# Kernel tuning notes

Hardware: AMD Instinct MI355X
Metric: run time of the kernel (lower is better)

## Reference

```python
import jax, jax.numpy as jnp
import numpy as np

MIN_NORM = 1e-15
BALL_EPS = 4e-3  # hgcn PoincareBall eps for float32
C = 1.0          # c_in = c_out = 1


def _artanh(x):
    return jnp.arctanh(jnp.clip(x, -1.0 + 1e-7, 1.0 - 1e-7))


def _norm(x):
    return jnp.clip(jnp.linalg.norm(x, axis=-1, keepdims=True), MIN_NORM)


def proj(x, c=C):
    n = _norm(x)
    maxnorm = (1.0 - BALL_EPS) / jnp.sqrt(c)
    return jnp.where(n > maxnorm, x / n * maxnorm, x)


def expmap0(u, c=C):
    sc = jnp.sqrt(c)
    n = _norm(u)
    return jnp.tanh(sc * n) * u / (sc * n)


def logmap0(p, c=C):
    sc = jnp.sqrt(c)
    n = _norm(p)
    return _artanh(sc * n) * p / (sc * n)


def mobius_add(x, y, c=C):
    x2 = jnp.sum(x * x, -1, keepdims=True)
    y2 = jnp.sum(y * y, -1, keepdims=True)
    xy = jnp.sum(x * y, -1, keepdims=True)
    num = (1 + 2 * c * xy + c * y2) * x + (1 - c * x2) * y
    den = 1 + 2 * c * xy + c * c * x2 * y2
    return num / jnp.clip(den, MIN_NORM)


def mobius_matvec(m, x, c=C):
    # m: [out, in] torch-Linear layout; mx = x @ m.T
    sc = jnp.sqrt(c)
    xn = _norm(x)
    mx = x @ m.T
    mxn = _norm(mx)
    res = jnp.tanh(mxn / xn * _artanh(sc * xn)) * mx / (mxn * sc)
    zero = jnp.all(mx == 0, axis=-1, keepdims=True)
    return jnp.where(zero, jnp.zeros_like(res), res)


def hyp_linear(x, w, b, c=C):
    res = proj(mobius_matvec(w, x, c), c)
    hyp_bias = proj(expmap0(b[None, :], c), c)  # proj_tan0 is identity on Poincare ball
    return proj(mobius_add(res, hyp_bias, c), c)


def hyp_act(x, c_in=C, c_out=C):
    xt = jax.nn.relu(logmap0(x, c_in))
    return proj(expmap0(xt, c_out), c_out)


def mean_agg(h, src, dst, n):
    # mean of source-node features over incoming edges per destination node
    s = jax.ops.segment_sum(h[src], dst, num_segments=n)
    deg = jax.ops.segment_sum(jnp.ones((src.shape[0],), h.dtype), dst, num_segments=n)
    return s / jnp.clip(deg, 1.0)[:, None]


def setup_inputs() -> dict:
    key = jax.random.key(0)
    N, D, E = 100000, 128, 1600000  # in_features = out_features = 128
    ks = jax.random.split(key, 20)
    inp = {
        "x": jax.random.normal(ks[0], (N, D), jnp.float32) * 0.01,  # keep near ball origin
        "src_pos": jax.random.randint(ks[1], (E,), 0, N, jnp.int32),
        "dst_pos": jax.random.randint(ks[2], (E,), 0, N, jnp.int32),
        "src_neg": jax.random.randint(ks[3], (E,), 0, N, jnp.int32),
        "dst_neg": jax.random.randint(ks[4], (E,), 0, N, jnp.int32),
    }
    s = 0.01
    inp["W1b"] = jax.random.normal(ks[5], (D, 2 * D), jnp.float32) * s
    inp["b1b"] = jax.random.normal(ks[6], (D,), jnp.float32) * s
    inp["W1h"] = jax.random.normal(ks[7], (D, 2 * D), jnp.float32) * s
    inp["b1h"] = jax.random.normal(ks[8], (D,), jnp.float32) * s
    inp["W2b"] = jax.random.normal(ks[9], (2 * D, 3 * D), jnp.float32) * s
    inp["b2b"] = jax.random.normal(ks[10], (2 * D,), jnp.float32) * s
    inp["W2h"] = jax.random.normal(ks[11], (2 * D, 3 * D), jnp.float32) * s
    inp["b2h"] = jax.random.normal(ks[12], (2 * D,), jnp.float32) * s
    inp["W3b"] = jax.random.normal(ks[13], (D, 2 * D), jnp.float32) * s
    inp["b3b"] = jax.random.normal(ks[14], (D,), jnp.float32) * s
    inp["W3h"] = jax.random.normal(ks[15], (D, 2 * D), jnp.float32) * s
    inp["b3h"] = jax.random.normal(ks[16], (D,), jnp.float32) * s
    return inp


def reference(x, src_pos, dst_pos, src_neg, dst_neg,
              W1b, b1b, W1h, b1h, W2b, b2b, W2h, b2h, W3b, b3b, W3h, b3h):
    n = x.shape[0]
    # layer-1 signed neighbor means over x
    pos1 = mean_agg(x, src_pos, dst_pos, n)
    neg1 = mean_agg(x, src_neg, dst_neg, n)
    h_b1 = hyp_act(hyp_linear(jnp.concatenate([pos1, x], axis=1), W1b, b1b))
    h_n1 = hyp_act(hyp_linear(jnp.concatenate([neg1, x], axis=1), W1h, b1h))
    # layer-2 balance-theory aggregation over (h_b1, h_n1)
    pos2 = jnp.concatenate([mean_agg(h_b1, src_pos, dst_pos, n),
                            mean_agg(h_n1, src_neg, dst_neg, n)], axis=1)
    neg2 = jnp.concatenate([mean_agg(h_n1, src_pos, dst_pos, n),
                            mean_agg(h_b1, src_neg, dst_neg, n)], axis=1)
    h_b2 = hyp_act(hyp_linear(jnp.concatenate([pos2, h_b1], axis=1), W2b, b2b))
    h_n2 = hyp_act(hyp_linear(jnp.concatenate([neg2, h_n1], axis=1), W2h, b2h))
    h_b3 = hyp_act(hyp_linear(h_b2, W3b, b3b))
    h_n3 = hyp_act(hyp_linear(h_n2, W3h, b3h))
    return jnp.concatenate([h_b3, h_n3, x], axis=1)  # [N, 3*D]
```

## Files before the change

kernel.cpp:

```cpp
#include <hip/hip_runtime.h>
#include <cstdint>
#include <cstddef>

#define DEV __device__ __forceinline__

typedef unsigned int uint32;
typedef unsigned short ushort16;
typedef __bf16 bfx8 __attribute__((ext_vector_type(8)));
typedef float f32x4 __attribute__((ext_vector_type(4)));

constexpr int D = 128;
constexpr int CAP = 64;
constexpr float MINN  = 1e-15f;
constexpr float MAXN  = 1.0f - 4e-3f;
constexpr float ACLIP = 1.0f - 1e-7f;

DEV float wave_sum(float v) {
#pragma unroll
  for (int off = 32; off > 0; off >>= 1) v += __shfl_xor(v, off, 64);
  return v;
}

DEV float artanh_clip(float x) {
  x = fminf(x, ACLIP);
  return 0.5f * logf((1.0f + x) / (1.0f - x));
}

DEV uint32 f2b(float f) {
  uint32 u = __float_as_uint(f);
  u += 0x7fffu + ((u >> 16) & 1u);
  return u >> 16;
}
DEV float b2f_lo(uint32 v) { return __uint_as_float(v << 16); }
DEV float b2f_hi(uint32 v) { return __uint_as_float(v & 0xffff0000u); }

__global__ __launch_bounds__(256) void fillc_k(
    const int* __restrict__ sp, const int* __restrict__ dp,
    const int* __restrict__ sn, const int* __restrict__ dn, int E,
    int* __restrict__ cp, int* __restrict__ cn,
    int* __restrict__ lp, int* __restrict__ ln, int rngsz, int chunkE) {
  const int* __restrict__ src = blockIdx.y ? sn : sp;
  const int* __restrict__ dst = blockIdx.y ? dn : dp;
  int* __restrict__ cur = blockIdx.y ? cn : cp;
  int* __restrict__ lst = blockIdx.y ? ln : lp;
  const int r = blockIdx.x & 7;
  const int chunk = blockIdx.x >> 3;
  const unsigned lo = (unsigned)(r * rngsz);
  const int base = chunk * chunkE;
  const int end = min(base + chunkE, E);
  for (int i = base + (int)threadIdx.x; i < end; i += 256) {
    int d = dst[i];
    if ((unsigned)d - lo < (unsigned)rngsz) {
      int p = atomicAdd(&cur[d], 1);
      if (p < CAP) lst[(size_t)d * CAP + p] = src[i];
    }
  }
}

__global__ void rowsq_k(const float* __restrict__ x, float* __restrict__ xsq,
                        ushort16* __restrict__ xb, float* __restrict__ outx,
                        int* __restrict__ curz, int nz, int n) {
  int gid = blockIdx.x * 256 + (int)threadIdx.x;
  if (gid < nz) curz[gid] = 0;
  int lane = threadIdx.x & 63;
  int row = blockIdx.x * 4 + (threadIdx.x >> 6);
  if (row >= n) return;
  const float2 v = *(const float2*)(x + (size_t)row * D + lane * 2);
  uint32 pk = f2b(v.x) | (f2b(v.y) << 16);
  *(uint32*)(xb + (size_t)row * D + lane * 2) = pk;
  *(float2*)(outx + (size_t)row * 384 + 256 + lane * 2) = v;
  float s = wave_sum(v.x * v.x + v.y * v.y);
  if (lane == 0) xsq[row] = s;
}

struct BiasDesc { const float* b[6]; float* hb[6]; int dim[6]; };
__global__ void bias_all_k(BiasDesc bd, float* __restrict__ hbsq) {
  int i = blockIdx.x;
  int lane = threadIdx.x;
  const float* b = bd.b[i];
  float* hb = bd.hb[i];
  int ne = bd.dim[i] / 64;
  float v[4];
  float ssq = 0.0f;
  for (int e = 0; e < ne; ++e) { v[e] = b[e * 64 + lane]; ssq += v[e] * v[e]; }
  ssq = wave_sum(ssq);
  float nr = sqrtf(ssq);
  float nc = fmaxf(nr, MINN);
  float es = tanhf(nc) / nc;
  float on = es * nr;
  float f = (on > MAXN) ? (MAXN / fmaxf(on, MINN)) : 1.0f;
  float w = es * f;
  float osq = 0.0f;
  for (int e = 0; e < ne; ++e) { v[e] *= w; osq += v[e] * v[e]; hb[e * 64 + lane] = v[e]; }
  osq = wave_sum(osq);
  if (lane == 0) hbsq[i] = osq;
}

struct WsDesc { const float* src[6]; ushort16* dst[6]; int K[6]; int total[6]; };
__global__ void wshuf_all_k(WsDesc wd) {
  int y = blockIdx.y;
  int tid = blockIdx.x * 256 + threadIdx.x;
  if (tid >= wd.total[y]) return;
  int K = wd.K[y];
  int l = tid & 63;
  int fc = tid >> 6;
  int nkc = K / 32;
  int kc = fc % nkc;
  int jt = fc / nkc;
  int col = jt * 16 + (l & 15);
  int kb = kc * 32 + (l >> 4) * 8;
  const float* src = wd.src[y] + (size_t)col * K + kb;
  uint32 o[4];
#pragma unroll
  for (int m = 0; m < 4; ++m) o[m] = f2b(src[2 * m]) | (f2b(src[2 * m + 1]) << 16);
  *(uint4*)(wd.dst[y] + (size_t)tid * 8) = make_uint4(o[0], o[1], o[2], o[3]);
}

struct AggJob {
  const char* T;
  const int* cnt; const int* lst;
  ushort16* OutLo; ushort16* OutHi;
  float* Slo; float* Shi;
};

template <int NF>
__global__ __launch_bounds__(256) void agg2_k(AggJob ja, AggJob jbv, int n) {
  AggJob jb = blockIdx.y ? jbv : ja;
  const int l = threadIdx.x & 63;
  const int row = blockIdx.x * 4 + ((int)threadIdx.x >> 6);
  if (row >= n) return;
  const int cnt = jb.cnt[row];
  const int m = min(cnt, CAP);
  const int* __restrict__ lst = jb.lst + (size_t)row * CAP;
  const char* __restrict__ T = jb.T;
  float a0 = 0, a1 = 0, a2 = 0, a3 = 0;
  int j = 0;
  if (NF == 2) {
    const int off = l * 8;
    for (; j + 15 < m; j += 16) {
      uint2 v[16];
#pragma unroll
      for (int q = 0; q < 16; ++q)
        v[q] = *(const uint2*)(T + (size_t)lst[j + q] * 512 + off);
#pragma unroll
      for (int q = 0; q < 16; ++q) {
        a0 += b2f_lo(v[q].x); a1 += b2f_hi(v[q].x);
        a2 += b2f_lo(v[q].y); a3 += b2f_hi(v[q].y);
      }
    }
    for (; j + 3 < m; j += 4) {
      uint2 v[4];
#pragma unroll
      for (int q = 0; q < 4; ++q)
        v[q] = *(const uint2*)(T + (size_t)lst[j + q] * 512 + off);
#pragma unroll
      for (int q = 0; q < 4; ++q) {
        a0 += b2f_lo(v[q].x); a1 += b2f_hi(v[q].x);
        a2 += b2f_lo(v[q].y); a3 += b2f_hi(v[q].y);
      }
    }
    for (; j < m; ++j) {
      uint2 v = *(const uint2*)(T + (size_t)lst[j] * 512 + off);
      a0 += b2f_lo(v.x); a1 += b2f_hi(v.x);
      a2 += b2f_lo(v.y); a3 += b2f_hi(v.y);
    }
  } else {
    const int off = (l & 31) * 8;
    const int g = l >> 5;
    for (; j + 15 < m; j += 16) {
      uint2 v[8];
#pragma unroll
      for (int q = 0; q < 8; ++q)
        v[q] = *(const uint2*)(T + (size_t)lst[j + g + 2 * q] * 256 + off);
#pragma unroll
      for (int q = 0; q < 8; ++q) {
        a0 += b2f_lo(v[q].x); a1 += b2f_hi(v[q].x);
        a2 += b2f_lo(v[q].y); a3 += b2f_hi(v[q].y);
      }
    }
    for (; j + 1 < m; j += 2) {
      uint2 v = *(const uint2*)(T + (size_t)lst[j + g] * 256 + off);
      a0 += b2f_lo(v.x); a1 += b2f_hi(v.x);
      a2 += b2f_lo(v.y); a3 += b2f_hi(v.y);
    }
    if (j < m && g == 0) {
      uint2 v = *(const uint2*)(T + (size_t)lst[j] * 256 + off);
      a0 += b2f_lo(v.x); a1 += b2f_hi(v.x);
      a2 += b2f_lo(v.y); a3 += b2f_hi(v.y);
    }
    a0 += __shfl_xor(a0, 32, 64);
    a1 += __shfl_xor(a1, 32, 64);
    a2 += __shfl_xor(a2, 32, 64);
    a3 += __shfl_xor(a3, 32, 64);
  }
  float inv = 1.0f / fmaxf((float)cnt, 1.0f);
  a0 *= inv; a1 *= inv; a2 *= inv; a3 *= inv;
  float sq = a0 * a0 + a1 * a1 + a2 * a2 + a3 * a3;
#pragma unroll
  for (int o2 = 1; o2 < 32; o2 <<= 1) sq += __shfl_xor(sq, o2, 64);
  uint2 o;
  o.x = f2b(a0) | (f2b(a1) << 16);
  o.y = f2b(a2) | (f2b(a3) << 16);
  if (NF == 2) {
    ushort16* Out = (l < 32) ? jb.OutLo : jb.OutHi;
    *(uint2*)((char*)Out + (size_t)row * 256 + (l & 31) * 8) = o;
    if (l == 0) jb.Slo[row] = sq;
    if (l == 32) jb.Shi[row] = sq;
  } else {
    if (l < 32) *(uint2*)((char*)jb.OutLo + (size_t)row * 256 + l * 8) = o;
    if (l == 0) jb.Slo[row] = sq;
  }
}

struct GJob {
  const ushort16* p[3];
  int lda[3], ko[3];
  const ushort16* Wp;
  const float *xs0, *xs1, *xs2;
  const float *hb, *hbsq_p;
  ushort16 *ob0, *ob1; int ldob;
  float* outf; int ldof, ocol;
  float* hsq_out;
};

template <int NC, int NCT>
__global__ __launch_bounds__(256) void gemm3_k(GJob j0, GJob j1, int M) {
  GJob jb = blockIdx.y ? j1 : j0;
  __shared__ char As[16384];
  __shared__ float hbs[NCT * 64];
  __shared__ float redA[4][64][2];
  __shared__ float redB[4][64];
  __shared__ float rs[64][4];
  const int t = threadIdx.x;
  const int l = t & 63;
  const int w = t >> 6;
  const int brow = blockIdx.x * 64;
  constexpr int KC32 = NC * 4;
  const int srow = t >> 4;
  const int sco = t & 15;

  for (int c = t; c < NCT * 64; c += 256) hbs[c] = jb.hb[c];

  auto gaddr = [&](int c, int h) -> const uint4* {
    int gr = min(brow + srow + h * 16, M - 1);
    return (const uint4*)(jb.p[c] + jb.ko[c] + (size_t)gr * jb.lda[c] + sco * 8);
  };

  f32x4 acc[4][NCT] = {};
  uint4 rga[4];
#pragma unroll
  for (int h = 0; h < 4; ++h) rga[h] = *gaddr(0, h);

#pragma unroll
  for (int c = 0; c < NC; ++c) {
#pragma unroll
    for (int h = 0; h < 4; ++h) {
      int row = srow + h * 16;
      *(uint4*)(As + row * 256 + ((sco * 16) ^ ((row & 7) << 4))) = rga[h];
    }
    __syncthreads();
    if (c + 1 < NC) {
#pragma unroll
      for (int h = 0; h < 4; ++h) rga[h] = *gaddr(c + 1, h);
    }
#pragma unroll
    for (int ks = 0; ks < 4; ++ks) {
      const int kb = ks * 64 + (l >> 4) * 16;
      bfx8 a[4], b[NCT];
#pragma unroll
      for (int j = 0; j < NCT; ++j)
        b[j] = *(const bfx8*)(jb.Wp + ((size_t)((w * NCT + j) * KC32 + c * 4 + ks)) * 512 + l * 8);
#pragma unroll
      for (int i = 0; i < 4; ++i) {
        int row = i * 16 + (l & 15);
        a[i] = *(const bfx8*)(As + row * 256 + (kb ^ ((row & 7) << 4)));
      }
#pragma unroll
      for (int i = 0; i < 4; ++i)
#pragma unroll
        for (int j = 0; j < NCT; ++j)
          acc[i][j] = __builtin_amdgcn_mfma_f32_16x16x32_bf16(a[i], b[j], acc[i][j], 0, 0, 0);
    }
    __syncthreads();
  }

#pragma unroll
  for (int i = 0; i < 4; ++i)
#pragma unroll
    for (int r = 0; r < 4; ++r) {
      float s = 0.0f, xy = 0.0f;
#pragma unroll
      for (int j = 0; j < NCT; ++j) {
        float m = acc[i][j][r];
        int col = w * (NCT * 16) + j * 16 + (l & 15);
        s += m * m;
        xy += m * hbs[col];
      }
#pragma unroll
      for (int off = 1; off < 16; off <<= 1) {
        s += __shfl_xor(s, off, 64);
        xy += __shfl_xor(xy, off, 64);
      }
      if ((l & 15) == 0) {
        int row = i * 16 + (l >> 4) * 4 + r;
        redA[w][row][0] = s;
        redA[w][row][1] = xy;
      }
    }
  __syncthreads();

  if (t < 64 && brow + t < M) {
    float ssq = redA[0][t][0] + redA[1][t][0] + redA[2][t][0] + redA[3][t][0];
    float xyr = redA[0][t][1] + redA[1][t][1] + redA[2][t][1] + redA[3][t][1];
    float mxn_raw = sqrtf(ssq);
    float xnsq = jb.xs0[brow + t];
    if (jb.xs1) xnsq += jb.xs1[brow + t];
    if (jb.xs2) xnsq += jb.xs2[brow + t];
    float xn = fmaxf(sqrtf(xnsq), MINN);
    float mxn = fmaxf(mxn_raw, MINN);
    float scal = tanhf(mxn / xn * artanh_clip(xn)) / mxn;
    float rn_raw = scal * mxn_raw;
    if (rn_raw > MAXN) { scal *= MAXN / fmaxf(rn_raw, MINN); rn_raw = MAXN; }
    float xyv = scal * xyr;
    float x2 = rn_raw * rn_raw;
    float y2 = *jb.hbsq_p;
    float den = fmaxf(1.0f + 2.0f * xyv + x2 * y2, MINN);
    float ax = (1.0f + 2.0f * xyv + y2) / den;
    float ay = (1.0f - x2) / den;
    float vsq = scal * scal * ssq;
    float psq = fmaxf(ax * ax * vsq + 2.0f * ax * ay * xyv + ay * ay * y2, 0.0f);
    float pn_raw = sqrtf(psq);
    float f2s = (pn_raw > MAXN) ? (MAXN / fmaxf(pn_raw, MINN)) : 1.0f;
    pn_raw = fminf(pn_raw, MAXN);
    float pn = fmaxf(pn_raw, MINN);
    float la = artanh_clip(pn) / pn * f2s;
    rs[t][0] = scal * ax;
    rs[t][1] = ay;
    rs[t][2] = la;
  }
  __syncthreads();

#pragma unroll
  for (int i = 0; i < 4; ++i)
#pragma unroll
    for (int r = 0; r < 4; ++r) {
      int row = i * 16 + (l >> 4) * 4 + r;
      float c1 = rs[row][0], c2 = rs[row][1];
      float pp = 0.0f;
#pragma unroll
      for (int j = 0; j < NCT; ++j) {
        int col = w * (NCT * 16) + j * 16 + (l & 15);
        float p = c1 * acc[i][j][r] + c2 * hbs[col];
        p = fmaxf(p, 0.0f);
        acc[i][j][r] = p;
        pp += p * p;
      }
#pragma unroll
      for (int off = 1; off < 16; off <<= 1) pp += __shfl_xor(pp, off, 64);
      if ((l & 15) == 0) redB[w][row] = pp;
    }
  __syncthreads();

  if (t < 64 && brow + t < M) {
    float ppos = redB[0][t] + redB[1][t] + redB[2][t] + redB[3][t];
    float la = rs[t][2];
    float tsq = la * la * ppos;
    float tn_raw = sqrtf(tsq);
    float tnc = fmaxf(tn_raw, MINN);
    float es = tanhf(tnc) / tnc;
    float on_raw = es * tn_raw;
    float f3 = (on_raw > MAXN) ? (MAXN / fmaxf(on_raw, MINN)) : 1.0f;
    float wsc = es * f3;
    float g = wsc * la;
    rs[t][3] = g;
    if (jb.hsq_out) jb.hsq_out[brow + t] = g * g * ppos;
  }
  __syncthreads();

#pragma unroll
  for (int i = 0; i < 4; ++i)
#pragma unroll
    for (int r = 0; r < 4; ++r) {
      int row = i * 16 + (l >> 4) * 4 + r;
      int gr = brow + row;
      if (gr < M) {
        float g = rs[row][3];
#pragma unroll
        for (int j = 0; j < NCT; ++j) {
          int col = w * (NCT * 16) + j * 16 + (l & 15);
          float o = g * acc[i][j][r];
          if (jb.ob0) {
            ushort16* ob = (col < 128) ? jb.ob0 : jb.ob1;
            ob[(size_t)gr * jb.ldob + (col & 127)] = (ushort16)f2b(o);
          } else {
            jb.outf[(size_t)gr * jb.ldof + jb.ocol + col] = o;
          }
        }
      }
    }
}

extern "C" void kernel_launch(void* const* d_in, const int* in_sizes, int n_in,
                              void* d_out, int out_size, void* d_ws, size_t ws_size,
                              hipStream_t stream) {
  const float* x = (const float*)d_in[0];
  const int* src_pos = (const int*)d_in[1];
  const int* dst_pos = (const int*)d_in[2];
  const int* src_neg = (const int*)d_in[3];
  const int* dst_neg = (const int*)d_in[4];
  const float* W1b = (const float*)d_in[5];
  const float* b1b = (const float*)d_in[6];
  const float* W1h = (const float*)d_in[7];
  const float* b1h = (const float*)d_in[8];
  const float* W2b = (const float*)d_in[9];
  const float* b2b = (const float*)d_in[10];
  const float* W2h = (const float*)d_in[11];
  const float* b2h = (const float*)d_in[12];
  const float* W3b = (const float*)d_in[13];
  const float* b3b = (const float*)d_in[14];
  const float* W3h = (const float*)d_in[15];
  const float* b3h = (const float*)d_in[16];

  const int N = in_sizes[0] / D;
  const int E = in_sizes[1];

  int* iw = (int*)d_ws;
  size_t io = 0;
  int* cur_p = iw + io;  io += N;
  int* cur_n = iw + io;  io += N;
  int* lst_p = iw + io;  io += (size_t)N * CAP;
  int* lst_n = iw + io;  io += (size_t)N * CAP;
  io = (io + 63) & ~(size_t)63;

  float* fw = (float*)(iw + io);
  size_t fo = 0;
  float* xsq = fw + fo;    fo += N;
  float* hsq_b1 = fw + fo; fo += N;
  float* hsq_n1 = fw + fo; fo += N;
  float* hsq_b2 = fw + fo; fo += N;
  float* hsq_n2 = fw + fo; fo += N;
  float* ssq_p1 = fw + fo; fo += N;
  float* ssq_n1 = fw + fo; fo += N;
  float* ssq_pp = fw + fo; fo += N;
  float* ssq_np = fw + fo; fo += N;
  float* ssq_nn = fw + fo; fo += N;
  float* ssq_bn = fw + fo; fo += N;
  float* hbase = fw + fo;  fo += 1056;
  fo = (fo + 31) & ~(size_t)31;

  ushort16* SB = (ushort16*)(fw + fo);
  const size_t NSB = (size_t)N * D;
  ushort16* TA = SB;
  ushort16* H1 = SB + NSB;
  ushort16* TD = SB + 3 * NSB;
  ushort16* TE = SB + 4 * NSB;
  ushort16* TF = SB + 5 * NSB;
  ushort16* wb1b = SB + 6 * NSB;
  ushort16* wb1h = wb1b + 32768;
  ushort16* wb2b = wb1h + 32768;
  ushort16* wb2h = wb2b + 98304;
  ushort16* wb3b = wb2h + 98304;
  ushort16* wb3h = wb3b + 32768;

  float* outf = (float*)d_out;

  float* hb1b = hbase + 0;
  float* hb1h = hbase + 128;
  float* hb2b = hbase + 256;
  float* hb2h = hbase + 512;
  float* hb3b = hbase + 768;
  float* hb3h = hbase + 896;
  float* hbsq = hbase + 1024;

  const int grow = (N + 3) / 4;
  const int gf = (N + 63) / 64;
  const int rngsz = (N + 7) / 8;
  const int chunkE = (E + 255) / 256;
  const int gpart = 256 * 8;

  rowsq_k<<<grow, 256, 0, stream>>>(x, xsq, TA, outf, cur_p, 2 * N, N);
  fillc_k<<<dim3(gpart, 2), 256, 0, stream>>>(src_pos, dst_pos, src_neg, dst_neg, E,
                                              cur_p, cur_n, lst_p, lst_n, rngsz, chunkE);
  {
    BiasDesc bd;
    bd.b[0] = b1b; bd.hb[0] = hb1b; bd.dim[0] = 128;
    bd.b[1] = b1h; bd.hb[1] = hb1h; bd.dim[1] = 128;
    bd.b[2] = b2b; bd.hb[2] = hb2b; bd.dim[2] = 256;
    bd.b[3] = b2h; bd.hb[3] = hb2h; bd.dim[3] = 256;
    bd.b[4] = b3b; bd.hb[4] = hb3b; bd.dim[4] = 128;
    bd.b[5] = b3h; bd.hb[5] = hb3h; bd.dim[5] = 128;
    bias_all_k<<<6, 64, 0, stream>>>(bd, hbsq);
  }
  {
    WsDesc wd;
    wd.src[0] = W1b; wd.dst[0] = wb1b; wd.K[0] = 256; wd.total[0] = 8 * 8 * 64;
    wd.src[1] = W1h; wd.dst[1] = wb1h; wd.K[1] = 256; wd.total[1] = 8 * 8 * 64;
    wd.src[2] = W2b; wd.dst[2] = wb2b; wd.K[2] = 384; wd.total[2] = 16 * 12 * 64;
    wd.src[3] = W2h; wd.dst[3] = wb2h; wd.K[3] = 384; wd.total[3] = 16 * 12 * 64;
    wd.src[4] = W3b; wd.dst[4] = wb3b; wd.K[4] = 256; wd.total[4] = 8 * 8 * 64;
    wd.src[5] = W3h; wd.dst[5] = wb3h; wd.K[5] = 256; wd.total[5] = 8 * 8 * 64;
    wshuf_all_k<<<dim3(48, 6), 256, 0, stream>>>(wd);
  }

  {
    AggJob jp{(const char*)TA, cur_p, lst_p, TD, nullptr, ssq_p1, nullptr};
    AggJob jn{(const char*)TA, cur_n, lst_n, TE, nullptr, ssq_n1, nullptr};
    agg2_k<1><<<dim3(grow, 2), 256, 0, stream>>>(jp, jn, N);
  }
  {
    GJob ja{}, jh{};
    ja.p[0] = TD; ja.lda[0] = 128; ja.ko[0] = 0;
    ja.p[1] = TA; ja.lda[1] = 128; ja.ko[1] = 0;
    ja.Wp = wb1b; ja.xs0 = ssq_p1; ja.xs1 = xsq; ja.xs2 = nullptr;
    ja.hb = hb1b; ja.hbsq_p = hbsq + 0;
    ja.ob0 = H1; ja.ob1 = nullptr; ja.ldob = 256;
    ja.outf = nullptr; ja.ldof = 0; ja.ocol = 0; ja.hsq_out = hsq_b1;
    jh = ja;
    jh.p[0] = TE; jh.Wp = wb1h; jh.xs0 = ssq_n1;
    jh.hb = hb1h; jh.hbsq_p = hbsq + 1; jh.ob0 = H1 + 128; jh.hsq_out = hsq_n1;
    gemm3_k<2, 2><<<dim3(gf, 2), 256, 0, stream>>>(ja, jh, N);
  }

  {
    AggJob jp{(const char*)H1, cur_p, lst_p, TD, TE, ssq_pp, ssq_np};
    AggJob jn{(const char*)H1, cur_n, lst_n, TF, TA, ssq_bn, ssq_nn};
    agg2_k<2><<<dim3(grow, 2), 256, 0, stream>>>(jp, jn, N);
  }
  {
    GJob ja{}, jh{};
    ja.p[0] = TD; ja.lda[0] = 128; ja.ko[0] = 0;
    ja.p[1] = TA; ja.lda[1] = 128; ja.ko[1] = 0;
    ja.p[2] = H1; ja.lda[2] = 256; ja.ko[2] = 0;
    ja.Wp = wb2b; ja.xs0 = ssq_pp; ja.xs1 = ssq_nn; ja.xs2 = hsq_b1;
    ja.hb = hb2b; ja.hbsq_p = hbsq + 2;
    ja.ob0 = TD; ja.ob1 = TA; ja.ldob = 128;
    ja.outf = nullptr; ja.ldof = 0; ja.ocol = 0; ja.hsq_out = hsq_b2;
    jh = ja;
    jh.p[0] = TE; jh.p[1] = TF; jh.ko[2] = 128;
    jh.Wp = wb2h; jh.xs0 = ssq_np; jh.xs1 = ssq_bn; jh.xs2 = hsq_n1;
    jh.hb = hb2h; jh.hbsq_p = hbsq + 3;
    jh.ob0 = TE; jh.ob1 = TF; jh.hsq_out = hsq_n2;
    gemm3_k<3, 4><<<dim3(gf, 2), 256, 0, stream>>>(ja, jh, N);
  }

  {
    GJob ja{}, jh{};
    ja.p[0] = TD; ja.lda[0] = 128; ja.ko[0] = 0;
    ja.p[1] = TA; ja.lda[1] = 128; ja.ko[1] = 0;
    ja.Wp = wb3b; ja.xs0 = hsq_b2; ja.xs1 = nullptr; ja.xs2 = nullptr;
    ja.hb = hb3b; ja.hbsq_p = hbsq + 4;
    ja.ob0 = nullptr; ja.ob1 = nullptr; ja.ldob = 0;
    ja.outf = outf; ja.ldof = 3 * D; ja.ocol = 0; ja.hsq_out = nullptr;
    jh = ja;
    jh.p[0] = TE; jh.p[1] = TF;
    jh.Wp = wb3h; jh.xs0 = hsq_n2;
    jh.hb = hb3h; jh.hbsq_p = hbsq + 5; jh.ocol = 128;
    gemm3_k<2, 2><<<dim3(gf, 2), 256, 0, stream>>>(ja, jh, N);
  }
}
```

Baseline: 866.4 us.

## Split each aggregation row across two wavefronts with narrower per-lane loads

The gather-mean aggregation kernel now assigns two wavefronts to each destination row instead of one. For two-feature tables each wave handles one 128-wide half with 4-byte loads. For single-feature tables the two waves take alternating edges and combine partial sums through shared memory with a block barrier. The goal is more waves in flight to hide gather latency, at the cost of narrower loads, twice the edge-index reads, and an extra sync in the single-feature path.

Result: slower. 988.0 us (+14.0%).

```diff
diff --git a/kernel.cpp b/kernel.cpp
--- a/kernel.cpp
+++ b/kernel.cpp
@@ -127,87 +127,65 @@
 __global__ __launch_bounds__(256) void agg2_k(AggJob ja, AggJob jbv, int n) {
   AggJob jb = blockIdx.y ? jbv : ja;
   const int l = threadIdx.x & 63;
-  const int row = blockIdx.x * 4 + ((int)threadIdx.x >> 6);
-  if (row >= n) return;
-  const int cnt = jb.cnt[row];
-  const int m = min(cnt, CAP);
-  const int* __restrict__ lst = jb.lst + (size_t)row * CAP;
-  const char* __restrict__ T = jb.T;
-  float a0 = 0, a1 = 0, a2 = 0, a3 = 0;
-  int j = 0;
+  const int wv = (int)threadIdx.x >> 6;
+  const int row = blockIdx.x * 2 + (wv >> 1);
+  const int half = wv & 1;
   if (NF == 2) {
-    const int off = l * 8;
-    for (; j + 15 < m; j += 16) {
-      uint2 v[16];
-#pragma unroll
-      for (int q = 0; q < 16; ++q)
-        v[q] = *(const uint2*)(T + (size_t)lst[j + q] * 512 + off);
-#pragma unroll
-      for (int q = 0; q < 16; ++q) {
-        a0 += b2f_lo(v[q].x); a1 += b2f_hi(v[q].x);
-        a2 += b2f_lo(v[q].y); a3 += b2f_hi(v[q].y);
-      }
-    }
-    for (; j + 3 < m; j += 4) {
-      uint2 v[4];
-#pragma unroll
-      for (int q = 0; q < 4; ++q)
-        v[q] = *(const uint2*)(T + (size_t)lst[j + q] * 512 + off);
-#pragma unroll
-      for (int q = 0; q < 4; ++q) {
-        a0 += b2f_lo(v[q].x); a1 += b2f_hi(v[q].x);
-        a2 += b2f_lo(v[q].y); a3 += b2f_hi(v[q].y);
-      }
+    if (row >= n) return;
+    const int cnt = jb.cnt[row];
+    const int m = min(cnt, CAP);
+    const int* __restrict__ lst = jb.lst + (size_t)row * CAP;
+    const char* __restrict__ T = jb.T + half * 256 + l * 4;
+    float a0 = 0, a1 = 0;
+    int j = 0;
+    for (; j + 7 < m; j += 8) {
+      uint32 v[8];
+#pragma unroll
+      for (int q = 0; q < 8; ++q) v[q] = *(const uint32*)(T + (size_t)lst[j + q] * 512);
+#pragma unroll
+      for (int q = 0; q < 8; ++q) { a0 += b2f_lo(v[q]); a1 += b2f_hi(v[q]); }
     }
     for (; j < m; ++j) {
-      uint2 v = *(const uint2*)(T + (size_t)lst[j] * 512 + off);
-      a0 += b2f_lo(v.x); a1 += b2f_hi(v.x);
-      a2 += b2f_lo(v.y); a3 += b2f_hi(v.y);
-    }
+      uint32 v = *(const uint32*)(T + (size_t)lst[j] * 512);
+      a0 += b2f_lo(v); a1 += b2f_hi(v);
+    }
+    float inv = 1.0f / fmaxf((float)cnt, 1.0f);
+    a0 *= inv; a1 *= inv;
+    float sq = wave_sum(a0 * a0 + a1 * a1);
+    ushort16* Out = half ? jb.OutHi : jb.OutLo;
+    *(uint32*)((char*)Out + (size_t)row * 256 + l * 4) = f2b(a0) | (f2b(a1) << 16);
+    if (l == 0) (half ? jb.Shi : jb.Slo)[row] = sq;
   } else {
-    const int off = (l & 31) * 8;
-    const int g = l >> 5;
-    for (; j + 15 < m; j += 16) {
-      uint2 v[8];
-#pragma unroll
-      for (int q = 0; q < 8; ++q)
-        v[q] = *(const uint2*)(T + (size_t)lst[j + g + 2 * q] * 256 + off);
-#pragma unroll
-      for (int q = 0; q < 8; ++q) {
-        a0 += b2f_lo(v[q].x); a1 += b2f_hi(v[q].x);
-        a2 += b2f_lo(v[q].y); a3 += b2f_hi(v[q].y);
-      }
-    }
-    for (; j + 1 < m; j += 2) {
-      uint2 v = *(const uint2*)(T + (size_t)lst[j + g] * 256 + off);
-      a0 += b2f_lo(v.x); a1 += b2f_hi(v.x);
-      a2 += b2f_lo(v.y); a3 += b2f_hi(v.y);
-    }
-    if (j < m && g == 0) {
-      uint2 v = *(const uint2*)(T + (size_t)lst[j] * 256 + off);
-      a0 += b2f_lo(v.x); a1 += b2f_hi(v.x);
-      a2 += b2f_lo(v.y); a3 += b2f_hi(v.y);
-    }
-    a0 += __shfl_xor(a0, 32, 64);
-    a1 += __shfl_xor(a1, 32, 64);
-    a2 += __shfl_xor(a2, 32, 64);
-    a3 += __shfl_xor(a3, 32, 64);
-  }
-  float inv = 1.0f / fmaxf((float)cnt, 1.0f);
-  a0 *= inv; a1 *= inv; a2 *= inv; a3 *= inv;
-  float sq = a0 * a0 + a1 * a1 + a2 * a2 + a3 * a3;
-#pragma unroll
-  for (int o2 = 1; o2 < 32; o2 <<= 1) sq += __shfl_xor(sq, o2, 64);
-  uint2 o;
-  o.x = f2b(a0) | (f2b(a1) << 16);
-  o.y = f2b(a2) | (f2b(a3) << 16);
-  if (NF == 2) {
-    ushort16* Out = (l < 32) ? jb.OutLo : jb.OutHi;
-    *(uint2*)((char*)Out + (size_t)row * 256 + (l & 31) * 8) = o;
-    if (l == 0) jb.Slo[row] = sq;
-    if (l == 32) jb.Shi[row] = sq;
-  } else {
-    if (l < 32) *(uint2*)((char*)jb.OutLo + (size_t)row * 256 + l * 8) = o;
+    __shared__ float2 part[2][64];
+    const bool valid = row < n;
+    int cnt = 0, m = 0;
+    const int* __restrict__ lst = nullptr;
+    if (valid) { cnt = jb.cnt[row]; m = min(cnt, CAP); lst = jb.lst + (size_t)row * CAP; }
+    const char* __restrict__ T = jb.T + l * 4;
+    float a0 = 0, a1 = 0;
+    if (valid) {
+      int j = half;
+      for (; j + 14 < m; j += 16) {
+        uint32 v[8];
+#pragma unroll
+        for (int q = 0; q < 8; ++q) v[q] = *(const uint32*)(T + (size_t)lst[j + 2 * q] * 256);
+#pragma unroll
+        for (int q = 0; q < 8; ++q) { a0 += b2f_lo(v[q]); a1 += b2f_hi(v[q]); }
+      }
+      for (; j < m; j += 2) {
+        uint32 v = *(const uint32*)(T + (size_t)lst[j] * 256);
+        a0 += b2f_lo(v); a1 += b2f_hi(v);
+      }
+    }
+    if (half) part[wv >> 1][l] = make_float2(a0, a1);
+    __syncthreads();
+    if (!valid || half) return;
+    float2 p = part[wv >> 1][l];
+    a0 += p.x; a1 += p.y;
+    float inv = 1.0f / fmaxf((float)cnt, 1.0f);
+    a0 *= inv; a1 *= inv;
+    float sq = wave_sum(a0 * a0 + a1 * a1);
+    *(uint32*)((char*)jb.OutLo + (size_t)row * 256 + l * 4) = f2b(a0) | (f2b(a1) << 16);
     if (l == 0) jb.Slo[row] = sq;
   }
 }
@@ -473,6 +451,7 @@
   float* hbsq = hbase + 1024;
 
   const int grow = (N + 3) / 4;
+  const int grow2 = (N + 1) / 2;
   const int gf = (N + 63) / 64;
   const int rngsz = (N + 7) / 8;
   const int chunkE = (E + 255) / 256;
@@ -505,7 +484,7 @@
   {
     AggJob jp{(const char*)TA, cur_p, lst_p, TD, nullptr, ssq_p1, nullptr};
     AggJob jn{(const char*)TA, cur_n, lst_n, TE, nullptr, ssq_n1, nullptr};
-    agg2_k<1><<<dim3(grow, 2), 256, 0, stream>>>(jp, jn, N);
+    agg2_k<1><<<dim3(grow2, 2), 256, 0, stream>>>(jp, jn, N);
   }
   {
     GJob ja{}, jh{};
@@ -524,7 +503,7 @@
   {
     AggJob jp{(const char*)H1, cur_p, lst_p, TD, TE, ssq_pp, ssq_np};
     AggJob jn{(const char*)H1, cur_n, lst_n, TF, TA, ssq_bn, ssq_nn};
-    agg2_k<2><<<dim3(grow, 2), 256, 0, stream>>>(jp, jn, N);
+    agg2_k<2><<<dim3(grow2, 2), 256, 0, stream>>>(jp, jn, N);
   }
   {
     GJob ja{}, jh{};
```
